# Optimization experiments

Hardware: AMD Instinct MI355X
Metric: run time of the kernel (lower is better)

## Reference

```python
import jax, jax.numpy as jnp
import numpy as np

D = 512; H = 8; DH = D // H; FFN = 2048; K = 31; N = 4; T = 1024


def _ln(x, g, b):
    m = jnp.mean(x, -1, keepdims=True)
    v = jnp.var(x, -1, keepdims=True)
    return (x - m) * jax.lax.rsqrt(v + 1e-5) * g + b


def _ff(x, g, b, w1, b1, w2, b2):
    h = jax.nn.silu(_ln(x, g, b) @ w1 + b1)
    return 0.5 * (h @ w2 + b2)


def _forward(x, rel_pe, ln1_g, ln1_b, ff1_w1, ff1_b1, ff1_w2, ff1_b2,
             an_g, an_b, wq, bq, wk, bk, wv, bv, wo, bo, pos_w, u, v,
             cn_g, cn_b, pe_w, pe_b, dw_w, dw_b, bn_g, bn_b, pc_w, pc_b,
             ln2_g, ln2_b, ff2_w1, ff2_b1, ff2_w2, ff2_b2, fn_g, fn_b):
    Nb, Tt, _ = x.shape
    # macaron FF 1 (half-step)
    x = x + _ff(x, ln1_g, ln1_b, ff1_w1, ff1_b1, ff1_w2, ff1_b2)

    # RPE multi-head attention (Transformer-XL style)
    xa = _ln(x, an_g, an_b)
    split = lambda m: m.reshape(Nb, Tt, H, DH).transpose(0, 2, 1, 3)  # (N,H,T,dh)
    Q = split(xa @ wq + bq)
    Kk = split(xa @ wk + bk)
    V = split(xa @ wv + bv)
    # content-to-content: (Q+u) K^T
    AC = jnp.einsum('nhtd,nhsd->nhts', Q + u[None, :, None, :], Kk)
    # content-to-position: (Q+v) R^T, then rel-shift gather
    R = (rel_pe @ pos_w).reshape(2 * Tt - 1, H, DH)  # (2T-1,H,dh)
    BD_raw = jnp.einsum('nhtd,phd->nhtp', Q + v[None, :, None, :], R)  # (N,H,T,2T-1)
    idx = jnp.arange(Tt - 1, -1, -1)[None, :] + jnp.arange(Tt)[:, None]  # (T,T): i-j+(T-1)
    BD = jnp.take_along_axis(BD_raw, idx[None, None, :, :], axis=-1)  # (N,H,T,T)
    scores = (AC + BD) * (DH ** -0.5)
    attn = jax.nn.softmax(scores, axis=-1)
    out = jnp.einsum('nhts,nhsd->nthd', attn, V).reshape(Nb, Tt, D)
    x = x + (out @ wo + bo)

    # conv module: LN -> pointwise expand -> GLU -> depthwise conv -> BN(eval) -> SiLU -> pointwise
    c = _ln(x, cn_g, cn_b) @ pe_w + pe_b  # (N,T,2D)
    a, g = jnp.split(c, 2, axis=-1)
    c = a * jax.nn.sigmoid(g)
    c = c.transpose(0, 2, 1)  # (N,D,T)
    c = jax.lax.conv_general_dilated(
        c, dw_w, window_strides=(1,), padding=[(K // 2, K // 2)],
        dimension_numbers=('NCH', 'OIH', 'NCH'), feature_group_count=D)
    c = c + dw_b[None, :, None]
    # BatchNorm1d in eval mode: running_mean=0, running_var=1
    c = c * bn_g[None, :, None] + bn_b[None, :, None]
    c = jax.nn.silu(c).transpose(0, 2, 1) @ pc_w + pc_b
    x = x + c

    # macaron FF 2 + final LN
    x = x + _ff(x, ln2_g, ln2_b, ff2_w1, ff2_b1, ff2_w2, ff2_b2)
    return _ln(x, fn_g, fn_b)


def setup_inputs() -> dict:
    keys = iter(jax.random.split(jax.random.key(0), 64))
    def rn(*shape, s=0.02):
        return jax.random.normal(next(keys), shape, jnp.float32) * s
    inp = {}
    inp['x'] = rn(N, T, D, s=1.0)
    inp['rel_pe'] = rn(2 * T - 1, D, s=1.0)
    inp['ln1_g'] = jnp.ones(D); inp['ln1_b'] = jnp.zeros(D)
    inp['ff1_w1'] = rn(D, FFN); inp['ff1_b1'] = jnp.zeros(FFN)
    inp['ff1_w2'] = rn(FFN, D); inp['ff1_b2'] = jnp.zeros(D)
    inp['an_g'] = jnp.ones(D); inp['an_b'] = jnp.zeros(D)
    inp['wq'] = rn(D, D); inp['bq'] = jnp.zeros(D)
    inp['wk'] = rn(D, D); inp['bk'] = jnp.zeros(D)
    inp['wv'] = rn(D, D); inp['bv'] = jnp.zeros(D)
    inp['wo'] = rn(D, D); inp['bo'] = jnp.zeros(D)
    inp['pos_w'] = rn(D, D)
    inp['u'] = rn(H, DH); inp['v'] = rn(H, DH)
    inp['cn_g'] = jnp.ones(D); inp['cn_b'] = jnp.zeros(D)
    inp['pe_w'] = rn(D, 2 * D); inp['pe_b'] = jnp.zeros(2 * D)
    inp['dw_w'] = rn(D, 1, K); inp['dw_b'] = jnp.zeros(D)
    inp['bn_g'] = jnp.ones(D); inp['bn_b'] = jnp.zeros(D)
    inp['pc_w'] = rn(D, D); inp['pc_b'] = jnp.zeros(D)
    inp['ln2_g'] = jnp.ones(D); inp['ln2_b'] = jnp.zeros(D)
    inp['ff2_w1'] = rn(D, FFN); inp['ff2_b1'] = jnp.zeros(FFN)
    inp['ff2_w2'] = rn(FFN, D); inp['ff2_b2'] = jnp.zeros(D)
    inp['fn_g'] = jnp.ones(D); inp['fn_b'] = jnp.zeros(D)
    return inp


def reference(x, rel_pe, ln1_g, ln1_b, ff1_w1, ff1_b1, ff1_w2, ff1_b2,
              an_g, an_b, wq, bq, wk, bk, wv, bv, wo, bo, pos_w, u, v,
              cn_g, cn_b, pe_w, pe_b, dw_w, dw_b, bn_g, bn_b, pc_w, pc_b,
              ln2_g, ln2_b, ff2_w1, ff2_b1, ff2_w2, ff2_b2, fn_g, fn_b):
    return _forward(x, rel_pe, ln1_g, ln1_b, ff1_w1, ff1_b1, ff1_w2, ff1_b2,
                    an_g, an_b, wq, bq, wk, bk, wv, bv, wo, bo, pos_w, u, v,
                    cn_g, cn_b, pe_w, pe_b, dw_w, dw_b, bn_g, bn_b, pc_w, pc_b,
                    ln2_g, ln2_b, ff2_w1, ff2_b1, ff2_w2, ff2_b2, fn_g, fn_b)
```

## Files before the change

### kernel.cpp

```cpp
#include <hip/hip_runtime.h>
#include <hip/hip_bf16.h>

using bf16 = __hip_bfloat16;
typedef __attribute__((ext_vector_type(8))) short short8;
typedef __attribute__((ext_vector_type(4))) float f32x4;

static __device__ __forceinline__ float b2f(bf16 v) { return __bfloat162float(v); }
static __device__ __forceinline__ bf16  f2b(float v) { return __float2bfloat16(v); }
static __device__ __forceinline__ short f2bs(float x) {
    union { float f; unsigned u; } c; c.f = x;
    unsigned r = (c.u + 0x7FFFu + ((c.u >> 16) & 1u)) >> 16;
    return (short)r;
}
static __device__ __forceinline__ float bs2f(short s) {
    union { unsigned u; float f; } c; c.u = ((unsigned)(unsigned short)s) << 16;
    return c.f;
}

constexpr int kD   = 512;
constexpr int kT   = 1024;
constexpr int kN   = 4;
constexpr int kH   = 8;
constexpr int kDH  = 64;
constexpr int kFFN = 2048;
constexpr int kROWS = kN * kT;
constexpr int kP    = 2 * kT - 1;

#define ACT_NONE 0
#define ACT_SILU 1

__global__ __launch_bounds__(256) void stamp_kernel(float* __restrict__ out, int n, float val) {
    int i = blockIdx.x * 256 + threadIdx.x;
    if (i < n) out[i] = (i == 0 ? val : 0.f);
}

__global__ __launch_bounds__(256) void cvt_kernel(const float* __restrict__ in,
                                                  float* __restrict__ out, int n4) {
    int i = blockIdx.x * 256 + threadIdx.x;
    if (i < n4) ((f32x4*)out)[i] = ((const f32x4*)in)[i];
}

struct WtDesc { const float* src; short* dst; int K; int N; int tstart; };
struct WtArgs { WtDesc d[11]; };

__global__ __launch_bounds__(256) void wt_all_kernel(WtArgs a) {
    __shared__ float t[32][33];
    int bid = blockIdx.x;
    int i = 0;
#pragma unroll
    for (int j = 1; j < 11; ++j) if (bid >= a.d[j].tstart) i = j;
    const float* W = a.d[i].src;
    short* Wt = a.d[i].dst;
    int Kd = a.d[i].K, Nd = a.d[i].N;
    int lt = bid - a.d[i].tstart;
    int nx = Nd >> 5;
    int n0 = (lt % nx) * 32, k0 = (lt / nx) * 32;
    int tx = threadIdx.x & 31, ty = threadIdx.x >> 5;
#pragma unroll
    for (int it = 0; it < 4; ++it)
        t[ty + it * 8][tx] = W[(size_t)(k0 + ty + it * 8) * Nd + n0 + tx];
    __syncthreads();
#pragma unroll
    for (int it = 0; it < 4; ++it)
        Wt[(size_t)(n0 + ty + it * 8) * Kd + k0 + tx] = f2bs(t[tx][ty + it * 8]);
}

__global__ __launch_bounds__(256) void dwt_kernel(const float* __restrict__ dw_w,
                                                  const float* __restrict__ dw_b,
                                                  const float* __restrict__ bn_g,
                                                  const float* __restrict__ bn_b,
                                                  float* __restrict__ wt,
                                                  float* __restrict__ beff) {
    int idx = blockIdx.x * 256 + threadIdx.x;
    if (idx < 31 * kD) {
        int d = idx & 511, k = idx >> 9;
        wt[k * kD + d] = dw_w[d * 31 + k] * bn_g[d];
    }
    if (idx < kD) beff[idx] = dw_b[idx] * bn_g[idx] + bn_b[idx];
}

__global__ __launch_bounds__(256) void ln_kernel(const float* __restrict__ xin,
                                                 const float* __restrict__ g,
                                                 const float* __restrict__ b,
                                                 void* __restrict__ outp, int out_f32) {
    int row = blockIdx.x;
    const float* xr = xin + (size_t)row * kD;
    int tid = threadIdx.x;
    float v0 = xr[tid], v1 = xr[tid + 256];
    float s = v0 + v1, sq = v0 * v0 + v1 * v1;
    for (int off = 32; off; off >>= 1) {
        s  += __shfl_down(s, off);
        sq += __shfl_down(sq, off);
    }
    __shared__ float ss[4], ssq[4];
    __shared__ float mean_s, rstd_s;
    int wid = tid >> 6, lane = tid & 63;
    if (lane == 0) { ss[wid] = s; ssq[wid] = sq; }
    __syncthreads();
    if (tid == 0) {
        float S  = ss[0] + ss[1] + ss[2] + ss[3];
        float SQ = ssq[0] + ssq[1] + ssq[2] + ssq[3];
        float m = S / (float)kD;
        float var = SQ / (float)kD - m * m;
        mean_s = m;
        rstd_s = rsqrtf(fmaxf(var, 0.f) + 1e-5f);
    }
    __syncthreads();
    float m = mean_s, rs = rstd_s;
    float o0 = (v0 - m) * rs * g[tid]       + b[tid];
    float o1 = (v1 - m) * rs * g[tid + 256] + b[tid + 256];
    size_t i0 = (size_t)row * kD + tid, i1 = i0 + 256;
    if (out_f32) {
        ((float*)outp)[i0] = o0; ((float*)outp)[i1] = o1;
    } else {
        ((bf16*)outp)[i0] = f2b(o0); ((bf16*)outp)[i1] = f2b(o1);
    }
}

__global__ __launch_bounds__(256, 4) void gemm_mfma64(
    const void* __restrict__ A, const short* __restrict__ Bt,
    const float* __restrict__ bias, const float* __restrict__ residual,
    float* __restrict__ outf, bf16* __restrict__ outb,
    int M, int N, int K, int act, float scale, int a_f32) {
    __shared__ short As[64][72];
    __shared__ short Bs[64][72];
    int tid = threadIdx.x;
    int m0 = blockIdx.y * 64, n0 = blockIdx.x * 64;
    int wid = tid >> 6, lane = tid & 63;
    int wm = (wid >> 1) * 32, wn = (wid & 1) * 32;
    int q = lane >> 4, c16 = lane & 15;

    f32x4 zero4 = {0.f, 0.f, 0.f, 0.f};
    f32x4 acc[2][2] = {{zero4, zero4}, {zero4, zero4}};

    int srow = tid >> 3;
    int scol = (tid & 7) * 8;

    for (int k0 = 0; k0 < K; k0 += 64) {
        __syncthreads();
#pragma unroll
        for (int it = 0; it < 2; ++it) {
            int row = it * 32 + srow;
            int rr = m0 + row;
            short8 v = {0, 0, 0, 0, 0, 0, 0, 0};
            if (rr < M) {
                if (a_f32) {
                    const float* ap = (const float*)A + (size_t)rr * K + k0 + scol;
                    f32x4 x0 = *(const f32x4*)ap;
                    f32x4 x1 = *(const f32x4*)(ap + 4);
                    v[0] = f2bs(x0[0]); v[1] = f2bs(x0[1]); v[2] = f2bs(x0[2]); v[3] = f2bs(x0[3]);
                    v[4] = f2bs(x1[0]); v[5] = f2bs(x1[1]); v[6] = f2bs(x1[2]); v[7] = f2bs(x1[3]);
                } else {
                    v = *(const short8*)((const short*)A + (size_t)rr * K + k0 + scol);
                }
            }
            *(short8*)&As[row][scol] = v;
        }
#pragma unroll
        for (int it = 0; it < 2; ++it) {
            int row = it * 32 + srow;
            *(short8*)&Bs[row][scol] =
                *(const short8*)(Bt + (size_t)(n0 + row) * K + k0 + scol);
        }
        __syncthreads();
#pragma unroll
        for (int ks = 0; ks < 2; ++ks) {
            short8 af[2], bfr[2];
#pragma unroll
            for (int mt = 0; mt < 2; ++mt)
                af[mt] = *(const short8*)&As[wm + mt * 16 + c16][ks * 32 + q * 8];
#pragma unroll
            for (int nt = 0; nt < 2; ++nt)
                bfr[nt] = *(const short8*)&Bs[wn + nt * 16 + c16][ks * 32 + q * 8];
#pragma unroll
            for (int mt = 0; mt < 2; ++mt)
#pragma unroll
                for (int nt = 0; nt < 2; ++nt)
                    acc[mt][nt] = __builtin_amdgcn_mfma_f32_16x16x32_bf16(
                        af[mt], bfr[nt], acc[mt][nt], 0, 0, 0);
        }
    }
#pragma unroll
    for (int mt = 0; mt < 2; ++mt) {
#pragma unroll
        for (int reg = 0; reg < 4; ++reg) {
            int r = m0 + wm + mt * 16 + q * 4 + reg;
            if (r >= M) continue;
#pragma unroll
            for (int nt = 0; nt < 2; ++nt) {
                int c = n0 + wn + nt * 16 + c16;
                float h = acc[mt][nt][reg];
                if (bias) h += bias[c];
                if (act == ACT_SILU) h = h / (1.f + __expf(-h));
                h *= scale;
                size_t idx = (size_t)r * N + c;
                if (residual) h += residual[idx];
                if (outf) outf[idx] = h;
                if (outb) outb[idx] = f2b(h);
            }
        }
    }
}

__global__ __launch_bounds__(256, 4) void gemm_qkv(
    const bf16* __restrict__ A, const short* __restrict__ Bt,
    const float* __restrict__ bq, const float* __restrict__ bk,
    const float* __restrict__ bv,
    bf16* __restrict__ Qb, bf16* __restrict__ Kb, bf16* __restrict__ Vb) {
    const int K = kD;
    __shared__ short As[64][72];
    __shared__ short Bs[64][72];
    int tid = threadIdx.x;
    int m0 = blockIdx.y * 64, n0 = blockIdx.x * 64;
    int seg = blockIdx.x >> 3;
    const float* bias = seg == 0 ? bq : (seg == 1 ? bk : bv);
    bf16* outb = seg == 0 ? Qb : (seg == 1 ? Kb : Vb);
    int ns0 = n0 & 511;
    int wid = tid >> 6, lane = tid & 63;
    int wm = (wid >> 1) * 32, wn = (wid & 1) * 32;
    int q = lane >> 4, c16 = lane & 15;

    f32x4 zero4 = {0.f, 0.f, 0.f, 0.f};
    f32x4 acc[2][2] = {{zero4, zero4}, {zero4, zero4}};
    int srow = tid >> 3;
    int scol = (tid & 7) * 8;

    for (int k0 = 0; k0 < K; k0 += 64) {
        __syncthreads();
#pragma unroll
        for (int it = 0; it < 2; ++it) {
            int row = it * 32 + srow;
            *(short8*)&As[row][scol] =
                *(const short8*)((const short*)A + (size_t)(m0 + row) * K + k0 + scol);
            *(short8*)&Bs[row][scol] =
                *(const short8*)(Bt + (size_t)(n0 + row) * K + k0 + scol);
        }
        __syncthreads();
#pragma unroll
        for (int ks = 0; ks < 2; ++ks) {
            short8 af[2], bfr[2];
#pragma unroll
            for (int mt = 0; mt < 2; ++mt)
                af[mt] = *(const short8*)&As[wm + mt * 16 + c16][ks * 32 + q * 8];
#pragma unroll
            for (int nt = 0; nt < 2; ++nt)
                bfr[nt] = *(const short8*)&Bs[wn + nt * 16 + c16][ks * 32 + q * 8];
#pragma unroll
            for (int mt = 0; mt < 2; ++mt)
#pragma unroll
                for (int nt = 0; nt < 2; ++nt)
                    acc[mt][nt] = __builtin_amdgcn_mfma_f32_16x16x32_bf16(
                        af[mt], bfr[nt], acc[mt][nt], 0, 0, 0);
        }
    }
#pragma unroll
    for (int mt = 0; mt < 2; ++mt)
#pragma unroll
        for (int reg = 0; reg < 4; ++reg) {
            int r = m0 + wm + mt * 16 + q * 4 + reg;
#pragma unroll
            for (int nt = 0; nt < 2; ++nt) {
                int c = ns0 + wn + nt * 16 + c16;
                outb[(size_t)r * 512 + c] = f2b(acc[mt][nt][reg] + bias[c]);
            }
        }
}

__global__ __launch_bounds__(256) void gemm_scalar(
    const void* __restrict__ A, const float* __restrict__ W,
    const float* __restrict__ bias, const float* __restrict__ residual,
    float* __restrict__ outf, bf16* __restrict__ outb,
    int M, int N, int K, int act, float scale, int a_f32) {
    __shared__ float As[16][65];
    __shared__ float Bs[16][65];
    int tid = threadIdx.x;
    int tx = tid & 15, ty = tid >> 4;
    int row0 = blockIdx.y * 64, col0 = blockIdx.x * 64;
    float acc[4][4] = {};
    for (int k0 = 0; k0 < K; k0 += 16) {
        for (int i = tid; i < 64 * 16; i += 256) {
            int r = i >> 4, c = i & 15;
            int rr = row0 + r;
            float v = 0.f;
            if (rr < M) {
                size_t idx = (size_t)rr * K + k0 + c;
                v = a_f32 ? ((const float*)A)[idx] : b2f(((const bf16*)A)[idx]);
            }
            As[c][r] = v;
        }
        for (int i = tid; i < 16 * 64; i += 256) {
            int r = i >> 6, c = i & 63;
            Bs[r][c] = W[(size_t)(k0 + r) * N + col0 + c];
        }
        __syncthreads();
#pragma unroll
        for (int kk = 0; kk < 16; ++kk) {
            float a[4], b[4];
#pragma unroll
            for (int i = 0; i < 4; ++i) a[i] = As[kk][ty * 4 + i];
#pragma unroll
            for (int j = 0; j < 4; ++j) b[j] = Bs[kk][tx * 4 + j];
#pragma unroll
            for (int i = 0; i < 4; ++i)
#pragma unroll
                for (int j = 0; j < 4; ++j) acc[i][j] += a[i] * b[j];
        }
        __syncthreads();
    }
#pragma unroll
    for (int i = 0; i < 4; ++i) {
        int r = row0 + ty * 4 + i;
        if (r >= M) continue;
#pragma unroll
        for (int j = 0; j < 4; ++j) {
            int c = col0 + tx * 4 + j;
            float h = acc[i][j];
            if (bias) h += bias[c];
            if (act == ACT_SILU) h = h / (1.f + __expf(-h));
            h *= scale;
            size_t idx = (size_t)r * N + c;
            if (residual) h += residual[idx];
            if (outf) outf[idx] = h;
            if (outb) outb[idx] = f2b(h);
        }
    }
}

__global__ __launch_bounds__(256, 2) void attn_mfma(
    const bf16* __restrict__ Qg, const bf16* __restrict__ Kg,
    const bf16* __restrict__ Vg, const bf16* __restrict__ Rg,
    const float* __restrict__ uu, const float* __restrict__ vvp,
    bf16* __restrict__ outb) {
    __shared__ short Qu[64][72];
    __shared__ short Qv[64][72];
    __shared__ short Ks[64][72];
    __shared__ short Vt[64][72];
    __shared__ short Rw[128][72];
    __shared__ short Bp[64][136];

    int tid = threadIdx.x;
    int qb = blockIdx.x, h = blockIdx.y, n = blockIdx.z;
    int t0 = qb * 64;
    size_t baseq = ((size_t)n * kT) * 512 + (size_t)h * kDH;
    size_t baseo = ((size_t)n * kT) * kD + (size_t)h * kDH;

    int wid = tid >> 6, lane = tid & 63;
    int q = lane >> 4, c16 = lane & 15;
    int wm = wid * 16;
    int trow = wm + q * 4;

    {
        int t = tid >> 2, dg = (tid & 3) * 16;
        const short* qp = (const short*)Qg + baseq + (size_t)(t0 + t) * 512 + dg;
        short8 q0 = *(const short8*)qp;
        short8 q1 = *(const short8*)(qp + 8);
#pragma unroll
        for (int i = 0; i < 8; ++i) {
            float qv = bs2f(q0[i]);
            Qu[t][dg + i] = f2bs(qv + uu[h * 64 + dg + i]);
            Qv[t][dg + i] = f2bs(qv + vvp[h * 64 + dg + i]);
        }
#pragma unroll
        for (int i = 0; i < 8; ++i) {
            float qv = bs2f(q1[i]);
            Qu[t][dg + 8 + i] = f2bs(qv + uu[h * 64 + dg + 8 + i]);
            Qv[t][dg + 8 + i] = f2bs(qv + vvp[h * 64 + dg + 8 + i]);
        }
    }

    f32x4 zero4 = {0.f, 0.f, 0.f, 0.f};
    f32x4 acc_o[4] = {zero4, zero4, zero4, zero4};
    float m_i[4] = {-1e30f, -1e30f, -1e30f, -1e30f};
    float l_i[4] = {0.f, 0.f, 0.f, 0.f};

    for (int kt = 0; kt < 16; ++kt) {
        int s0 = kt * 64;
        __syncthreads();
        {
            int s = tid >> 2, dg = (tid & 3) * 16;
            const short* kp = (const short*)Kg + baseq + (size_t)(s0 + s) * 512 + dg;
            *(short8*)&Ks[s][dg]     = *(const short8*)kp;
            *(short8*)&Ks[s][dg + 8] = *(const short8*)(kp + 8);
            const short* vp = (const short*)Vg + baseq + (size_t)(s0 + s) * 512 + dg;
            short8 v0 = *(const short8*)vp;
            short8 v1 = *(const short8*)(vp + 8);
#pragma unroll
            for (int i = 0; i < 8; ++i) Vt[dg + i][s] = v0[i];
#pragma unroll
            for (int i = 0; i < 8; ++i) Vt[dg + 8 + i][s] = v1[i];
        }
        int p_base = t0 - s0 + 960;
#pragma unroll
        for (int it = 0; it < 4; ++it) {
            int i = tid + it * 256;
            int j = i >> 3, dg2 = (i & 7) * 8;
            int p = p_base + j;
            p = p < 0 ? 0 : (p > 2046 ? 2046 : p);
            *(short8*)&Rw[j][dg2] =
                *(const short8*)((const short*)Rg + (size_t)p * kD + h * kDH + dg2);
        }
        __syncthreads();

        f32x4 acc_s[4] = {zero4, zero4, zero4, zero4};
        f32x4 acc_b[8] = {zero4, zero4, zero4, zero4, zero4, zero4, zero4, zero4};
#pragma unroll
        for (int ks = 0; ks < 2; ++ks) {
            short8 au = *(const short8*)&Qu[wm + c16][ks * 32 + q * 8];
            short8 av = *(const short8*)&Qv[wm + c16][ks * 32 + q * 8];
#pragma unroll
            for (int nt = 0; nt < 4; ++nt) {
                short8 bk_ = *(const short8*)&Ks[nt * 16 + c16][ks * 32 + q * 8];
                acc_s[nt] = __builtin_amdgcn_mfma_f32_16x16x32_bf16(au, bk_, acc_s[nt], 0, 0, 0);
            }
#pragma unroll
            for (int jt = 0; jt < 8; ++jt) {
                short8 br_ = *(const short8*)&Rw[jt * 16 + c16][ks * 32 + q * 8];
                acc_b[jt] = __builtin_amdgcn_mfma_f32_16x16x32_bf16(av, br_, acc_b[jt], 0, 0, 0);
            }
        }
#pragma unroll
        for (int jt = 0; jt < 8; ++jt)
#pragma unroll
            for (int reg = 0; reg < 4; ++reg)
                Bp[trow + reg][jt * 16 + c16] = f2bs(acc_b[jt][reg]);

        float pmat[4][4];
        float alpha[4];
#pragma unroll
        for (int reg = 0; reg < 4; ++reg) {
            int t = trow + reg;
            float mrow = -1e30f;
#pragma unroll
            for (int nt = 0; nt < 4; ++nt) {
                int s = nt * 16 + c16;
                int j = t - s + 63;
                float sv = (acc_s[nt][reg] + bs2f(Bp[t][j])) * 0.125f;
                pmat[nt][reg] = sv;
                mrow = fmaxf(mrow, sv);
            }
            mrow = fmaxf(mrow, __shfl_xor(mrow, 1));
            mrow = fmaxf(mrow, __shfl_xor(mrow, 2));
            mrow = fmaxf(mrow, __shfl_xor(mrow, 4));
            mrow = fmaxf(mrow, __shfl_xor(mrow, 8));
            float m_new = fmaxf(m_i[reg], mrow);
            alpha[reg] = __expf(m_i[reg] - m_new);
            float ps = 0.f;
#pragma unroll
            for (int nt = 0; nt < 4; ++nt) {
                float pe = __expf(pmat[nt][reg] - m_new);
                pmat[nt][reg] = pe;
                ps += pe;
            }
            ps += __shfl_xor(ps, 1);
            ps += __shfl_xor(ps, 2);
            ps += __shfl_xor(ps, 4);
            ps += __shfl_xor(ps, 8);
            l_i[reg] = l_i[reg] * alpha[reg] + ps;
            m_i[reg] = m_new;
        }
#pragma unroll
        for (int nt = 0; nt < 4; ++nt)
#pragma unroll
            for (int reg = 0; reg < 4; ++reg)
                Bp[trow + reg][nt * 16 + c16] = f2bs(pmat[nt][reg]);
#pragma unroll
        for (int dt = 0; dt < 4; ++dt)
#pragma unroll
            for (int reg = 0; reg < 4; ++reg)
                acc_o[dt][reg] *= alpha[reg];
#pragma unroll
        for (int ks = 0; ks < 2; ++ks) {
            short8 ap = *(const short8*)&Bp[wm + c16][ks * 32 + q * 8];
#pragma unroll
            for (int dt = 0; dt < 4; ++dt) {
                short8 bv_ = *(const short8*)&Vt[dt * 16 + c16][ks * 32 + q * 8];
                acc_o[dt] = __builtin_amdgcn_mfma_f32_16x16x32_bf16(ap, bv_, acc_o[dt], 0, 0, 0);
            }
        }
    }
#pragma unroll
    for (int reg = 0; reg < 4; ++reg) {
        float inv = 1.f / l_i[reg];
        int t = trow + reg;
#pragma unroll
        for (int dt = 0; dt < 4; ++dt)
            outb[baseo + (size_t)(t0 + t) * kD + dt * 16 + c16] = f2b(acc_o[dt][reg] * inv);
    }
}

__global__ __launch_bounds__(256) void attn_kernel(
    const bf16* __restrict__ Qg, const bf16* __restrict__ Kg,
    const bf16* __restrict__ Vg, const bf16* __restrict__ Rg,
    const float* __restrict__ uu, const float* __restrict__ vvp,
    bf16* __restrict__ outb) {
    __shared__ float Qs[64][65];
    __shared__ bf16 Ps[64][66];
    __shared__ bf16 Ks[64][66];
    __shared__ bf16 Vs[64][66];
    __shared__ bf16 Rs[127][66];
    __shared__ float uf[64], vf[64];
    __shared__ float uK[64], vR[127];

    int tid = threadIdx.x;
    int qb = blockIdx.x, h = blockIdx.y, n = blockIdx.z;
    int t0 = qb * 64;
    size_t base = ((size_t)n * kT) * kD + (size_t)h * kDH;

    if (tid < 64) {
        uf[tid] = uu[h * 64 + tid];
        vf[tid] = vvp[h * 64 + tid];
    }
    for (int i = tid; i < 64 * 64; i += 256) {
        int r = i >> 6, d = i & 63;
        Qs[r][d] = b2f(Qg[base + (size_t)(t0 + r) * kD + d]);
    }
    int r = tid >> 2, seg = tid & 3;
    float m_i = -1e30f, l_i = 0.f;
    float Oa[16];
#pragma unroll
    for (int i = 0; i < 16; ++i) Oa[i] = 0.f;

    for (int kt = 0; kt < 16; ++kt) {
        int s0 = kt * 64;
        __syncthreads();
        for (int i = tid; i < 64 * 64; i += 256) {
            int s = i >> 6, d = i & 63;
            Ks[s][d] = Kg[base + (size_t)(s0 + s) * kD + d];
            Vs[s][d] = Vg[base + (size_t)(s0 + s) * kD + d];
        }
        int p_base = t0 - s0 + 960;
        for (int i = tid; i < 127 * 64; i += 256) {
            int j = i >> 6, d = i & 63;
            int p = p_base + j;
            p = p < 0 ? 0 : (p > 2046 ? 2046 : p);
            Rs[j][d] = Rg[(size_t)p * kD + h * kDH + d];
        }
        __syncthreads();
        if (tid < 64) {
            float s_ = 0.f;
            for (int d = 0; d < 64; ++d) s_ += uf[d] * b2f(Ks[tid][d]);
            uK[tid] = s_;
        } else if (tid < 64 + 127) {
            int j = tid - 64;
            float s_ = 0.f;
            for (int d = 0; d < 64; ++d) s_ += vf[d] * b2f(Rs[j][d]);
            vR[j] = s_;
        }
        __syncthreads();
        float sv[16];
        float smax = -1e30f;
#pragma unroll
        for (int jj = 0; jj < 16; ++jj) {
            int s = seg * 16 + jj;
            int j = r - s + 63;
            float acc = 0.f;
            for (int d = 0; d < 64; ++d)
                acc += Qs[r][d] * (b2f(Ks[s][d]) + b2f(Rs[j][d]));
            acc = (acc + uK[s] + vR[j]) * 0.125f;
            sv[jj] = acc;
            smax = fmaxf(smax, acc);
        }
        smax = fmaxf(smax, __shfl_xor(smax, 1));
        smax = fmaxf(smax, __shfl_xor(smax, 2));
        float m_new = fmaxf(m_i, smax);
        float alpha = __expf(m_i - m_new);
        float psum = 0.f;
#pragma unroll
        for (int jj = 0; jj < 16; ++jj) {
            float p = __expf(sv[jj] - m_new);
            Ps[r][seg * 16 + jj] = f2b(p);
            psum += p;
        }
        psum += __shfl_xor(psum, 1);
        psum += __shfl_xor(psum, 2);
        l_i = l_i * alpha + psum;
        m_i = m_new;
#pragma unroll
        for (int i = 0; i < 16; ++i) Oa[i] *= alpha;
        __syncthreads();
        for (int s = 0; s < 64; ++s) {
            float p = b2f(Ps[r][s]);
#pragma unroll
            for (int dd = 0; dd < 16; ++dd)
                Oa[dd] += p * b2f(Vs[s][seg * 16 + dd]);
        }
    }
    float inv = 1.f / l_i;
#pragma unroll
    for (int dd = 0; dd < 16; ++dd)
        outb[base + (size_t)(t0 + r) * kD + seg * 16 + dd] = f2b(Oa[dd] * inv);
}

__global__ __launch_bounds__(256) void glu_kernel_v(const bf16* __restrict__ c,
                                                    bf16* __restrict__ out) {
    int i8 = (blockIdx.x * 256 + threadIdx.x) * 8;
    int row = i8 >> 9, d = i8 & 511;
    const short* cp = (const short*)c + (size_t)row * 1024;
    short8 a8 = *(const short8*)(cp + d);
    short8 g8 = *(const short8*)(cp + 512 + d);
    short8 o;
#pragma unroll
    for (int i = 0; i < 8; ++i) {
        float a = bs2f(a8[i]), g = bs2f(g8[i]);
        o[i] = f2bs(a / (1.f + __expf(-g)));
    }
    *(short8*)((short*)out + i8) = o;
}

__global__ __launch_bounds__(256) void gluconv_kernel(
    const bf16* __restrict__ cbuf, const float* __restrict__ wt,
    const float* __restrict__ beff, bf16* __restrict__ outb) {
    __shared__ short gsm[94][72];
    __shared__ float wsm[31][64];
    __shared__ float bsm[64];
    int tid = threadIdx.x;
    int dg0 = blockIdx.x * 64;
    int t0  = blockIdx.y * 64;
    int n   = blockIdx.z;

#pragma unroll
    for (int it = 0; it < 3; ++it) {
        int idx = tid + it * 256;
        if (idx < 94 * 8) {
            int row = idx >> 3, cg = (idx & 7) * 8;
            int t = t0 - 15 + row;
            short8 o = {0, 0, 0, 0, 0, 0, 0, 0};
            if ((unsigned)t < (unsigned)kT) {
                const short* cp = (const short*)cbuf + ((size_t)n * kT + t) * 1024 + dg0 + cg;
                short8 a8 = *(const short8*)cp;
                short8 g8 = *(const short8*)(cp + 512);
#pragma unroll
                for (int i = 0; i < 8; ++i)
                    o[i] = f2bs(bs2f(a8[i]) / (1.f + __expf(-bs2f(g8[i]))));
            }
            *(short8*)&gsm[row][cg] = o;
        }
    }
#pragma unroll
    for (int it = 0; it < 8; ++it) {
        int i = tid + it * 256;
        if (i < 31 * 64) wsm[i >> 6][i & 63] = wt[(i >> 6) * kD + dg0 + (i & 63)];
    }
    if (tid < 64) bsm[tid] = beff[dg0 + tid];
    __syncthreads();

    int tl = tid >> 2, dgl = (tid & 3) * 16;
    float acc[16] = {};
#pragma unroll
    for (int k = 0; k < 31; ++k) {
        short8 g0 = *(const short8*)&gsm[tl + k][dgl];
        short8 g1 = *(const short8*)&gsm[tl + k][dgl + 8];
#pragma unroll
        for (int i = 0; i < 8; ++i) {
            acc[i]     += bs2f(g0[i]) * wsm[k][dgl + i];
            acc[8 + i] += bs2f(g1[i]) * wsm[k][dgl + 8 + i];
        }
    }
    short8 o0, o1;
#pragma unroll
    for (int i = 0; i < 8; ++i) {
        float h = acc[i] + bsm[dgl + i];
        o0[i] = f2bs(h / (1.f + __expf(-h)));
        h = acc[8 + i] + bsm[dgl + 8 + i];
        o1[i] = f2bs(h / (1.f + __expf(-h)));
    }
    short* op = (short*)outb + ((size_t)n * kT + t0 + tl) * kD + dg0 + dgl;
    *(short8*)op = o0;
    *(short8*)(op + 8) = o1;
}

__global__ __launch_bounds__(256) void conv_kernel(
    const bf16* __restrict__ glu, const float* __restrict__ dw_w,
    const float* __restrict__ dw_b, const float* __restrict__ bn_g,
    const float* __restrict__ bn_b, bf16* __restrict__ outb) {
    int idx = blockIdx.x * 256 + threadIdx.x;
    int d = idx & 511;
    int t = (idx >> 9) & 1023;
    int n = idx >> 19;
    const bf16* gp = glu + ((size_t)n * kT) * kD + d;
    float acc = 0.f;
#pragma unroll
    for (int k = 0; k < 31; ++k) {
        int tt = t + k - 15;
        if ((unsigned)tt < (unsigned)kT)
            acc += b2f(gp[(size_t)tt * kD]) * dw_w[d * 31 + k];
    }
    acc += dw_b[d];
    acc = acc * bn_g[d] + bn_b[d];
    acc = acc / (1.f + __expf(-acc));
    outb[idx] = f2b(acc);
}

extern "C" void kernel_launch(void* const* d_in, const int* in_sizes, int n_in,
                              void* d_out, int out_size, void* d_ws, size_t ws_size,
                              hipStream_t stream) {
    const float* x      = (const float*)d_in[0];
    const float* rel_pe = (const float*)d_in[1];
    const float* ln1_g  = (const float*)d_in[2];
    const float* ln1_b  = (const float*)d_in[3];
    const float* ff1_w1 = (const float*)d_in[4];
    const float* ff1_b1 = (const float*)d_in[5];
    const float* ff1_w2 = (const float*)d_in[6];
    const float* ff1_b2 = (const float*)d_in[7];
    const float* an_g   = (const float*)d_in[8];
    const float* an_b   = (const float*)d_in[9];
    const float* wq = (const float*)d_in[10]; const float* bq = (const float*)d_in[11];
    const float* wk = (const float*)d_in[12]; const float* bk = (const float*)d_in[13];
    const float* wv = (const float*)d_in[14]; const float* bv = (const float*)d_in[15];
    const float* wo = (const float*)d_in[16]; const float* bo = (const float*)d_in[17];
    const float* pos_w = (const float*)d_in[18];
    const float* uu = (const float*)d_in[19]; const float* vvp = (const float*)d_in[20];
    const float* cn_g = (const float*)d_in[21]; const float* cn_b = (const float*)d_in[22];
    const float* pe_w = (const float*)d_in[23]; const float* pe_b = (const float*)d_in[24];
    const float* dw_w = (const float*)d_in[25]; const float* dw_b = (const float*)d_in[26];
    const float* bn_g = (const float*)d_in[27]; const float* bn_b = (const float*)d_in[28];
    const float* pc_w = (const float*)d_in[29]; const float* pc_b = (const float*)d_in[30];
    const float* ln2_g = (const float*)d_in[31]; const float* ln2_b = (const float*)d_in[32];
    const float* ff2_w1 = (const float*)d_in[33]; const float* ff2_b1 = (const float*)d_in[34];
    const float* ff2_w2 = (const float*)d_in[35]; const float* ff2_b2 = (const float*)d_in[36];
    const float* fn_g = (const float*)d_in[37]; const float* fn_b = (const float*)d_in[38];
    (void)n_in; (void)in_sizes;

    const int total = kROWS * kD;
    dim3 blk(256);
    const size_t MB = 1ull << 20;
    char* w = (char*)d_ws;

    if (ws_size >= 30 * MB) {
        float* xf      = (float*)(w);
        short* ff1_w1t = (short*)(w + 8 * MB);
        short* ff1_w2t = (short*)(w + 10 * MB);
        short* wqt     = (short*)(w + 12 * MB);
        short* wkt     = (short*)(w + 12 * MB + 512 * 1024);
        short* wvt     = (short*)(w + 13 * MB);
        short* wot     = (short*)(w + 13 * MB + 512 * 1024);
        short* poswt   = (short*)(w + 14 * MB);
        short* pewt    = (short*)(w + 14 * MB + 512 * 1024);
        short* pcwt    = (short*)(w + 15 * MB + 512 * 1024);
        short* ff2_w1t = (short*)(w + 16 * MB);
        short* ff2_w2t = (short*)(w + 18 * MB);
        char*  dyn     = w + 20 * MB;
        bf16* hchunk = (bf16*)dyn;
        bf16* Qb     = (bf16*)dyn;
        bf16* Kb     = (bf16*)(dyn + 4 * MB);
        bf16* Rb     = (bf16*)(dyn + 8 * MB);
        bf16* cbuf   = (bf16*)dyn;
        float* dwt   = (float*)(dyn + 8 * MB);
        float* beff  = (float*)(dyn + 8 * MB + 256 * 1024);
        bf16* nb     = (bf16*)d_out;
        bf16* attnb  = (bf16*)d_out;
        bf16* convb  = (bf16*)d_out;
        bf16* Vb     = (bf16*)d_out + (size_t)kROWS * kD;

        WtArgs wa;
        const float* srcs[11] = {ff1_w1, ff1_w2, wq, wk, wv, wo, pos_w, pe_w, pc_w, ff2_w1, ff2_w2};
        short* dsts[11] = {ff1_w1t, ff1_w2t, wqt, wkt, wvt, wot, poswt, pewt, pcwt, ff2_w1t, ff2_w2t};
        int Ks_[11] = {512, 2048, 512, 512, 512, 512, 512, 512, 512, 512, 2048};
        int Ns_[11] = {2048, 512, 512, 512, 512, 512, 512, 1024, 512, 2048, 512};
        int cum = 0;
        for (int i = 0; i < 11; ++i) {
            wa.d[i].src = srcs[i]; wa.d[i].dst = dsts[i];
            wa.d[i].K = Ks_[i]; wa.d[i].N = Ns_[i]; wa.d[i].tstart = cum;
            cum += (Ns_[i] / 32) * (Ks_[i] / 32);
        }
        wt_all_kernel<<<cum, blk, 0, stream>>>(wa);

        ln_kernel<<<kROWS, blk, 0, stream>>>(x, ln1_g, ln1_b, nb, 0);
        for (int c = 0; c < 2; ++c) {
            size_t off = (size_t)c * 2048 * kD;
            gemm_mfma64<<<dim3(kFFN / 64, 2048 / 64), blk, 0, stream>>>(
                nb + off, ff1_w1t, ff1_b1, nullptr, nullptr, hchunk,
                2048, kFFN, kD, ACT_SILU, 1.f, 0);
            gemm_mfma64<<<dim3(kD / 64, 2048 / 64), blk, 0, stream>>>(
                hchunk, ff1_w2t, ff1_b2, x + off, xf + off, nullptr,
                2048, kD, kFFN, ACT_NONE, 0.5f, 0);
        }

        ln_kernel<<<kROWS, blk, 0, stream>>>(xf, an_g, an_b, nb, 0);
        gemm_qkv<<<dim3(24, kROWS / 64), blk, 0, stream>>>(
            nb, wqt, bq, bk, bv, Qb, Kb, Vb);
        gemm_mfma64<<<dim3(kD / 64, (kP + 63) / 64), blk, 0, stream>>>(
            rel_pe, poswt, nullptr, nullptr, nullptr, Rb, kP, kD, kD, ACT_NONE, 1.f, 1);
        attn_mfma<<<dim3(kT / 64, kH, kN), blk, 0, stream>>>(Qb, Kb, Vb, Rb, uu, vvp, attnb);
        gemm_mfma64<<<dim3(kD / 64, kROWS / 64), blk, 0, stream>>>(
            attnb, wot, bo, xf, xf, nullptr, kROWS, kD, kD, ACT_NONE, 1.f, 0);

        dwt_kernel<<<62, blk, 0, stream>>>(dw_w, dw_b, bn_g, bn_b, dwt, beff);
        ln_kernel<<<kROWS, blk, 0, stream>>>(xf, cn_g, cn_b, nb, 0);
        gemm_mfma64<<<dim3(2 * kD / 64, kROWS / 64), blk, 0, stream>>>(
            nb, pewt, pe_b, nullptr, nullptr, cbuf, kROWS, 2 * kD, kD, ACT_NONE, 1.f, 0);
        gluconv_kernel<<<dim3(8, 16, 4), blk, 0, stream>>>(cbuf, dwt, beff, convb);
        gemm_mfma64<<<dim3(kD / 64, kROWS / 64), blk, 0, stream>>>(
            convb, pcwt, pc_b, xf, xf, nullptr, kROWS, kD, kD, ACT_NONE, 1.f, 0);

        ln_kernel<<<kROWS, blk, 0, stream>>>(xf, ln2_g, ln2_b, nb, 0);
        for (int c = 0; c < 2; ++c) {
            size_t off = (size_t)c * 2048 * kD;
            gemm_mfma64<<<dim3(kFFN / 64, 2048 / 64), blk, 0, stream>>>(
                nb + off, ff2_w1t, ff2_b1, nullptr, nullptr, hchunk,
                2048, kFFN, kD, ACT_SILU, 1.f, 0);
            gemm_mfma64<<<dim3(kD / 64, 2048 / 64), blk, 0, stream>>>(
                hchunk, ff2_w2t, ff2_b2, xf + off, xf + off, nullptr,
                2048, kD, kFFN, ACT_NONE, 0.5f, 0);
        }

        ln_kernel<<<kROWS, blk, 0, stream>>>(xf, fn_g, fn_b, d_out, 1);
        return;
    }

    if (ws_size < 22 * MB) {
        stamp_kernel<<<(out_size + 255) / 256, blk, 0, stream>>>(
            (float*)d_out, out_size, 1000.f + (float)(ws_size / MB));
        return;
    }

    float* xf    = (float*)(w);
    bf16*  hbch  = (bf16*)(w + 8 * MB);
    bf16*  Qb    = (bf16*)(w + 8 * MB);
    bf16*  cbuf  = (bf16*)(w + 8 * MB);
    bf16*  convb = (bf16*)(w + 8 * MB);
    bf16*  Kb    = (bf16*)(w + 12 * MB);
    bf16*  Vb    = (bf16*)(w + 16 * MB);
    bf16*  glub  = (bf16*)(w + 16 * MB);
    bf16*  Rb    = (bf16*)(w + 20 * MB);
    bf16*  nb    = (bf16*)d_out;
    bf16*  attnb = (bf16*)d_out;

    cvt_kernel<<<total / 1024, blk, 0, stream>>>(x, xf, total / 4);

    ln_kernel<<<kROWS, blk, 0, stream>>>(xf, ln1_g, ln1_b, nb, 0);
    for (int c = 0; c < 4; ++c) {
        size_t off = (size_t)c * 1024 * kD;
        gemm_scalar<<<dim3(kFFN / 64, 1024 / 64), blk, 0, stream>>>(
            nb + off, ff1_w1, ff1_b1, nullptr, nullptr, hbch, 1024, kFFN, kD, ACT_SILU, 1.f, 0);
        gemm_scalar<<<dim3(kD / 64, 1024 / 64), blk, 0, stream>>>(
            hbch, ff1_w2, ff1_b2, xf + off, xf + off, nullptr, 1024, kD, kFFN, ACT_NONE, 0.5f, 0);
    }

    ln_kernel<<<kROWS, blk, 0, stream>>>(xf, an_g, an_b, nb, 0);
    gemm_scalar<<<dim3(kD / 64, kROWS / 64), blk, 0, stream>>>(
        nb, wq, bq, nullptr, nullptr, Qb, kROWS, kD, kD, ACT_NONE, 1.f, 0);
    gemm_scalar<<<dim3(kD / 64, kROWS / 64), blk, 0, stream>>>(
        nb, wk, bk, nullptr, nullptr, Kb, kROWS, kD, kD, ACT_NONE, 1.f, 0);
    gemm_scalar<<<dim3(kD / 64, kROWS / 64), blk, 0, stream>>>(
        nb, wv, bv, nullptr, nullptr, Vb, kROWS, kD, kD, ACT_NONE, 1.f, 0);
    gemm_scalar<<<dim3(kD / 64, (kP + 63) / 64), blk, 0, stream>>>(
        rel_pe, pos_w, nullptr, nullptr, nullptr, Rb, kP, kD, kD, ACT_NONE, 1.f, 1);
    attn_kernel<<<dim3(kT / 64, kH, kN), blk, 0, stream>>>(Qb, Kb, Vb, Rb, uu, vvp, attnb);
    gemm_scalar<<<dim3(kD / 64, kROWS / 64), blk, 0, stream>>>(
        attnb, wo, bo, xf, xf, nullptr, kROWS, kD, kD, ACT_NONE, 1.f, 0);

    ln_kernel<<<kROWS, blk, 0, stream>>>(xf, cn_g, cn_b, nb, 0);
    gemm_scalar<<<dim3(2 * kD / 64, kROWS / 64), blk, 0, stream>>>(
        nb, pe_w, pe_b, nullptr, nullptr, cbuf, kROWS, 2 * kD, kD, ACT_NONE, 1.f, 0);
    glu_kernel_v<<<total / 2048, blk, 0, stream>>>(cbuf, glub);
    conv_kernel<<<total / 256, blk, 0, stream>>>(glub, dw_w, dw_b, bn_g, bn_b, convb);
    gemm_scalar<<<dim3(kD / 64, kROWS / 64), blk, 0, stream>>>(
        convb, pc_w, pc_b, xf, xf, nullptr, kROWS, kD, kD, ACT_NONE, 1.f, 0);

    ln_kernel<<<kROWS, blk, 0, stream>>>(xf, ln2_g, ln2_b, nb, 0);
    for (int c = 0; c < 4; ++c) {
        size_t off = (size_t)c * 1024 * kD;
        gemm_scalar<<<dim3(kFFN / 64, 1024 / 64), blk, 0, stream>>>(
            nb + off, ff2_w1, ff2_b1, nullptr, nullptr, hbch, 1024, kFFN, kD, ACT_SILU, 1.f, 0);
        gemm_scalar<<<dim3(kD / 64, 1024 / 64), blk, 0, stream>>>(
            hbch, ff2_w2, ff2_b2, xf + off, xf + off, nullptr, 1024, kD, kFFN, ACT_NONE, 0.5f, 0);
    }

    ln_kernel<<<kROWS, blk, 0, stream>>>(xf, fn_g, fn_b, d_out, 1);
}
```

Baseline: 569.9 us.

## Use direct global-to-LDS loads with XOR swizzle and pre-transpose V for attention

The bf16 GEMM kernels now stage A and B tiles with global_load_lds 16-byte direct-to-LDS loads into an XOR-swizzled unpadded layout, removing the register round-trip and padding. A new vtrans kernel pre-transposes V per head so the attention kernel can load V^T with vector loads instead of scalar scattered LDS writes. Buffer aliasing is adjusted so attention output goes to the old V region. This adds an extra kernel launch and relies on M being a multiple of 64 for bf16 A inputs, since the bounds check is dropped.

```diff
diff --git a/kernel.cpp b/kernel.cpp
--- a/kernel.cpp
+++ b/kernel.cpp
@@ -15,6 +15,11 @@
 static __device__ __forceinline__ float bs2f(short s) {
     union { unsigned u; float f; } c; c.u = ((unsigned)(unsigned short)s) << 16;
     return c.f;
+}
+static __device__ __forceinline__ void gload16(const short* g, short* l) {
+    __builtin_amdgcn_global_load_lds(
+        (const __attribute__((address_space(1))) void*)g,
+        (__attribute__((address_space(3))) void*)l, 16, 0, 0);
 }
 
 constexpr int kD   = 512;
@@ -63,6 +68,29 @@
 #pragma unroll
     for (int it = 0; it < 4; ++it)
         Wt[(size_t)(n0 + ty + it * 8) * Kd + k0 + tx] = f2bs(t[tx][ty + it * 8]);
+}
+
+__global__ __launch_bounds__(256) void vtrans_kernel(const bf16* __restrict__ V,
+                                                     bf16* __restrict__ Vt) {
+    __shared__ short ts[64][72];
+    int tt = blockIdx.x, h = blockIdx.y, n = blockIdx.z;
+    int tid = threadIdx.x;
+    int r = tid >> 3, cg = (tid & 7) * 8;
+#pragma unroll
+    for (int it = 0; it < 2; ++it) {
+        int row = it * 32 + r;
+        *(short8*)&ts[row][cg] =
+            *(const short8*)((const short*)V + ((size_t)n * kT + tt * 64 + row) * 512 + h * 64 + cg);
+    }
+    __syncthreads();
+#pragma unroll
+    for (int it = 0; it < 2; ++it) {
+        int d = it * 32 + r;
+        short8 o;
+#pragma unroll
+        for (int i = 0; i < 8; ++i) o[i] = ts[cg + i][d];
+        *(short8*)((short*)Vt + ((size_t)(n * 8 + h) * 64 + d) * 1024 + tt * 64 + cg) = o;
+    }
 }
 
 __global__ __launch_bounds__(256) void dwt_kernel(const float* __restrict__ dw_w,
@@ -122,8 +150,8 @@
     const float* __restrict__ bias, const float* __restrict__ residual,
     float* __restrict__ outf, bf16* __restrict__ outb,
     int M, int N, int K, int act, float scale, int a_f32) {
-    __shared__ short As[64][72];
-    __shared__ short Bs[64][72];
+    __shared__ short As[4096];
+    __shared__ short Bs[4096];
     int tid = threadIdx.x;
     int m0 = blockIdx.y * 64, n0 = blockIdx.x * 64;
     int wid = tid >> 6, lane = tid & 63;
@@ -133,45 +161,56 @@
     f32x4 zero4 = {0.f, 0.f, 0.f, 0.f};
     f32x4 acc[2][2] = {{zero4, zero4}, {zero4, zero4}};
 
-    int srow = tid >> 3;
-    int scol = (tid & 7) * 8;
+    int arow = lane >> 3;
+    int aseg = (lane & 7) ^ arow;
 
     for (int k0 = 0; k0 < K; k0 += 64) {
         __syncthreads();
-#pragma unroll
-        for (int it = 0; it < 2; ++it) {
-            int row = it * 32 + srow;
-            int rr = m0 + row;
-            short8 v = {0, 0, 0, 0, 0, 0, 0, 0};
-            if (rr < M) {
-                if (a_f32) {
-                    const float* ap = (const float*)A + (size_t)rr * K + k0 + scol;
+        if (!a_f32) {
+#pragma unroll
+            for (int it = 0; it < 2; ++it) {
+                int rbase = (wid * 2 + it) * 8;
+                gload16((const short*)A + (size_t)(m0 + rbase + arow) * K + k0 + aseg * 8,
+                        As + (size_t)(wid * 2 + it) * 512);
+            }
+        } else {
+            int srow = tid >> 3, sseg = tid & 7;
+#pragma unroll
+            for (int it = 0; it < 2; ++it) {
+                int row = it * 32 + srow;
+                int rr = m0 + row;
+                short8 v = {0, 0, 0, 0, 0, 0, 0, 0};
+                if (rr < M) {
+                    const float* ap = (const float*)A + (size_t)rr * K + k0 + sseg * 8;
                     f32x4 x0 = *(const f32x4*)ap;
                     f32x4 x1 = *(const f32x4*)(ap + 4);
                     v[0] = f2bs(x0[0]); v[1] = f2bs(x0[1]); v[2] = f2bs(x0[2]); v[3] = f2bs(x0[3]);
                     v[4] = f2bs(x1[0]); v[5] = f2bs(x1[1]); v[6] = f2bs(x1[2]); v[7] = f2bs(x1[3]);
-                } else {
-                    v = *(const short8*)((const short*)A + (size_t)rr * K + k0 + scol);
                 }
-            }
-            *(short8*)&As[row][scol] = v;
+                *(short8*)&As[(row * 8 + (sseg ^ (row & 7))) * 8] = v;
+            }
         }
 #pragma unroll
         for (int it = 0; it < 2; ++it) {
-            int row = it * 32 + srow;
-            *(short8*)&Bs[row][scol] =
-                *(const short8*)(Bt + (size_t)(n0 + row) * K + k0 + scol);
+            int rbase = (wid * 2 + it) * 8;
+            gload16(Bt + (size_t)(n0 + rbase + arow) * K + k0 + aseg * 8,
+                    Bs + (size_t)(wid * 2 + it) * 512);
         }
         __syncthreads();
 #pragma unroll
         for (int ks = 0; ks < 2; ++ks) {
+            int p = c16 & 7;
             short8 af[2], bfr[2];
 #pragma unroll
-            for (int mt = 0; mt < 2; ++mt)
-                af[mt] = *(const short8*)&As[wm + mt * 16 + c16][ks * 32 + q * 8];
-#pragma unroll
-            for (int nt = 0; nt < 2; ++nt)
-                bfr[nt] = *(const short8*)&Bs[wn + nt * 16 + c16][ks * 32 + q * 8];
+            for (int mt = 0; mt < 2; ++mt) {
+                int row = wm + mt * 16 + c16;
+                af[mt] = *(const short8*)&As[(row * 8 + ((ks * 4 + q) ^ p)) * 8];
+            }
+#pragma unroll
+            for (int nt = 0; nt < 2; ++nt) {
+                int row = wn + nt * 16 + c16;
+                bfr[nt] = *(const short8*)&Bs[(row * 8 + ((ks * 4 + q) ^ p)) * 8];
+            }
 #pragma unroll
             for (int mt = 0; mt < 2; ++mt)
 #pragma unroll
@@ -208,8 +247,8 @@
     const float* __restrict__ bv,
     bf16* __restrict__ Qb, bf16* __restrict__ Kb, bf16* __restrict__ Vb) {
     const int K = kD;
-    __shared__ short As[64][72];
-    __shared__ short Bs[64][72];
+    __shared__ short As[4096];
+    __shared__ short Bs[4096];
     int tid = threadIdx.x;
     int m0 = blockIdx.y * 64, n0 = blockIdx.x * 64;
     int seg = blockIdx.x >> 3;
@@ -222,29 +261,34 @@
 
     f32x4 zero4 = {0.f, 0.f, 0.f, 0.f};
     f32x4 acc[2][2] = {{zero4, zero4}, {zero4, zero4}};
-    int srow = tid >> 3;
-    int scol = (tid & 7) * 8;
+    int arow = lane >> 3;
+    int aseg = (lane & 7) ^ arow;
 
     for (int k0 = 0; k0 < K; k0 += 64) {
         __syncthreads();
 #pragma unroll
         for (int it = 0; it < 2; ++it) {
-            int row = it * 32 + srow;
-            *(short8*)&As[row][scol] =
-                *(const short8*)((const short*)A + (size_t)(m0 + row) * K + k0 + scol);
-            *(short8*)&Bs[row][scol] =
-                *(const short8*)(Bt + (size_t)(n0 + row) * K + k0 + scol);
+            int rbase = (wid * 2 + it) * 8;
+            gload16((const short*)A + (size_t)(m0 + rbase + arow) * K + k0 + aseg * 8,
+                    As + (size_t)(wid * 2 + it) * 512);
+            gload16(Bt + (size_t)(n0 + rbase + arow) * K + k0 + aseg * 8,
+                    Bs + (size_t)(wid * 2 + it) * 512);
         }
         __syncthreads();
 #pragma unroll
         for (int ks = 0; ks < 2; ++ks) {
+            int p = c16 & 7;
             short8 af[2], bfr[2];
 #pragma unroll
-            for (int mt = 0; mt < 2; ++mt)
-                af[mt] = *(const short8*)&As[wm + mt * 16 + c16][ks * 32 + q * 8];
-#pragma unroll
-            for (int nt = 0; nt < 2; ++nt)
-                bfr[nt] = *(const short8*)&Bs[wn + nt * 16 + c16][ks * 32 + q * 8];
+            for (int mt = 0; mt < 2; ++mt) {
+                int row = wm + mt * 16 + c16;
+                af[mt] = *(const short8*)&As[(row * 8 + ((ks * 4 + q) ^ p)) * 8];
+            }
+#pragma unroll
+            for (int nt = 0; nt < 2; ++nt) {
+                int row = wn + nt * 16 + c16;
+                bfr[nt] = *(const short8*)&Bs[(row * 8 + ((ks * 4 + q) ^ p)) * 8];
+            }
 #pragma unroll
             for (int mt = 0; mt < 2; ++mt)
 #pragma unroll
@@ -328,7 +372,7 @@
 
 __global__ __launch_bounds__(256, 2) void attn_mfma(
     const bf16* __restrict__ Qg, const bf16* __restrict__ Kg,
-    const bf16* __restrict__ Vg, const bf16* __restrict__ Rg,
+    const bf16* __restrict__ Vtg, const bf16* __restrict__ Rg,
     const float* __restrict__ uu, const float* __restrict__ vvp,
     bf16* __restrict__ outb) {
     __shared__ short Qu[64][72];
@@ -342,6 +386,7 @@
     int qb = blockIdx.x, h = blockIdx.y, n = blockIdx.z;
     int t0 = qb * 64;
     size_t baseq = ((size_t)n * kT) * 512 + (size_t)h * kDH;
+    size_t basev = ((size_t)(n * 8 + h) * 64) * 1024;
     size_t baseo = ((size_t)n * kT) * kD + (size_t)h * kDH;
 
     int wid = tid >> 6, lane = tid & 63;
@@ -381,13 +426,9 @@
             const short* kp = (const short*)Kg + baseq + (size_t)(s0 + s) * 512 + dg;
             *(short8*)&Ks[s][dg]     = *(const short8*)kp;
             *(short8*)&Ks[s][dg + 8] = *(const short8*)(kp + 8);
-            const short* vp = (const short*)Vg + baseq + (size_t)(s0 + s) * 512 + dg;
-            short8 v0 = *(const short8*)vp;
-            short8 v1 = *(const short8*)(vp + 8);
-#pragma unroll
-            for (int i = 0; i < 8; ++i) Vt[dg + i][s] = v0[i];
-#pragma unroll
-            for (int i = 0; i < 8; ++i) Vt[dg + 8 + i][s] = v1[i];
+            const short* vp = (const short*)Vtg + basev + (size_t)s * 1024 + s0 + dg;
+            *(short8*)&Vt[s][dg]     = *(const short8*)vp;
+            *(short8*)&Vt[s][dg + 8] = *(const short8*)(vp + 8);
         }
         int p_base = t0 - s0 + 960;
 #pragma unroll
@@ -748,9 +789,10 @@
         float* dwt   = (float*)(dyn + 8 * MB);
         float* beff  = (float*)(dyn + 8 * MB + 256 * 1024);
         bf16* nb     = (bf16*)d_out;
-        bf16* attnb  = (bf16*)d_out;
+        bf16* Vtg    = (bf16*)d_out;
         bf16* convb  = (bf16*)d_out;
         bf16* Vb     = (bf16*)d_out + (size_t)kROWS * kD;
+        bf16* attnb  = Vb;
 
         WtArgs wa;
         const float* srcs[11] = {ff1_w1, ff1_w2, wq, wk, wv, wo, pos_w, pe_w, pc_w, ff2_w1, ff2_w2};
@@ -779,9 +821,10 @@
         ln_kernel<<<kROWS, blk, 0, stream>>>(xf, an_g, an_b, nb, 0);
         gemm_qkv<<<dim3(24, kROWS / 64), blk, 0, stream>>>(
             nb, wqt, bq, bk, bv, Qb, Kb, Vb);
+        vtrans_kernel<<<dim3(16, 8, 4), blk, 0, stream>>>(Vb, Vtg);
         gemm_mfma64<<<dim3(kD / 64, (kP + 63) / 64), blk, 0, stream>>>(
             rel_pe, poswt, nullptr, nullptr, nullptr, Rb, kP, kD, kD, ACT_NONE, 1.f, 1);
-        attn_mfma<<<dim3(kT / 64, kH, kN), blk, 0, stream>>>(Qb, Kb, Vb, Rb, uu, vvp, attnb);
+        attn_mfma<<<dim3(kT / 64, kH, kN), blk, 0, stream>>>(Qb, Kb, Vtg, Rb, uu, vvp, attnb);
         gemm_mfma64<<<dim3(kD / 64, kROWS / 64), blk, 0, stream>>>(
             attnb, wot, bo, xf, xf, nullptr, kROWS, kD, kD, ACT_NONE, 1.f, 0);
 
```

Result: faster. 501.8 us (-12.0%).
